# Kernel optimization log

Measured on AMD Instinct MI355X. Metric: run time of the kernel, lower is better.

Reference implementation:

```python
import jax, jax.numpy as jnp
import numpy as np

D_MODEL = 1024
NUM_HEADS = 16
D_K = D_MODEL // NUM_HEADS
B, S = 2, 2048


def setup_inputs() -> dict:
    key = jax.random.key(0)
    ks = jax.random.split(key, 9)
    sc = 1.0 / np.sqrt(D_MODEL)
    return {
        "x": jax.random.normal(ks[0], (B, S, D_MODEL), dtype=jnp.float32),
        "Wq": jax.random.normal(ks[1], (D_MODEL, D_MODEL), dtype=jnp.float32) * sc,
        "bq": jnp.zeros((D_MODEL,), dtype=jnp.float32),
        "Wk": jax.random.normal(ks[2], (D_MODEL, D_MODEL), dtype=jnp.float32) * sc,
        "bk": jnp.zeros((D_MODEL,), dtype=jnp.float32),
        "Wv": jax.random.normal(ks[3], (D_MODEL, D_MODEL), dtype=jnp.float32) * sc,
        "bv": jnp.zeros((D_MODEL,), dtype=jnp.float32),
        "Wo": jax.random.normal(ks[4], (D_MODEL, D_MODEL), dtype=jnp.float32) * sc,
        "bo": jnpp if False else jnp.zeros((D_MODEL,), dtype=jnp.float32),
    }


def reference(x, Wq, bq, Wk, bk, Wv, bv, Wo, bo):
    b, s, d = x.shape
    # projections, split heads: (B, H, S, Dk)
    def heads(t):
        return t.reshape(b, s, NUM_HEADS, D_K).transpose(0, 2, 1, 3)
    Q = heads(x @ Wq + bq)
    K = heads(x @ Wk + bk)
    V = heads(x @ Wv + bv)
    scores = jnp.einsum("bhqd,bhkd->bhqk", Q, K) / jnp.sqrt(jnp.float32(D_K))
    attn = jax.nn.softmax(scores, axis=-1)
    out = jnp.einsum("bhqk,bhkd->bhqd", attn, V)
    out = out.transpose(0, 2, 1, 3).reshape(b, s, d)
    return out @ Wo + bo
```

## Files before the change

### kernel.cpp

```cpp
#include <hip/hip_runtime.h>
#include <hip/hip_bf16.h>


#define SEQ 2048
#define DMODEL 1024
#define NHEAD 16
#define DK 64
#define NBATCH 2
#define NBH 32
#define MTOT 4096

typedef __attribute__((ext_vector_type(4))) float  f32x4;
typedef __attribute__((ext_vector_type(8))) short  bf16x8;
typedef __attribute__((ext_vector_type(4))) short  bf16x4;
typedef __attribute__((ext_vector_type(4))) unsigned short u16x4;

#define QSCALE 0.18033688f

__device__ __forceinline__ unsigned short f2bf(float x) {
  union { __hip_bfloat16 h; unsigned short u; } cv;
  cv.h = __float2bfloat16(x);
  return cv.u;
}

#define EXP2(x) __builtin_amdgcn_exp2f(x)

__device__ __forceinline__ float fmax3(float a, float b, float c) {
  return fmaxf(fmaxf(a, b), c);
}

__device__ __forceinline__ void gload16(const void* g, void* l) {
  __builtin_amdgcn_global_load_lds(
      (const __attribute__((address_space(1))) unsigned int*)g,
      (__attribute__((address_space(3))) unsigned int*)l, 16, 0, 0);
}

__global__ __launch_bounds__(256) void conv_all(
    const float* __restrict__ X, unsigned short* __restrict__ Xb,
    const float* __restrict__ W0, const float* __restrict__ W1,
    const float* __restrict__ W2, const float* __restrict__ W3,
    unsigned short* __restrict__ T0, unsigned short* __restrict__ T1,
    unsigned short* __restrict__ T2, unsigned short* __restrict__ T3) {
  __shared__ float tile[64][65];
  const int b = blockIdx.x;
  if (b >= 1024) {
    size_t i = ((size_t)(b - 1024) * 256 + threadIdx.x) * 16;
#pragma unroll
    for (int c = 0; c < 4; ++c) {
      f32x4 v = *(const f32x4*)&X[i + c * 4];
      u16x4 pk;
      pk[0] = f2bf(v[0]); pk[1] = f2bf(v[1]);
      pk[2] = f2bf(v[2]); pk[3] = f2bf(v[3]);
      *(u16x4*)&Xb[i + c * 4] = pk;
    }
    return;
  }
  const int z = b >> 8, rem = b & 255;
  const float* W; unsigned short* T;
  switch (z) {
    case 0: W = W0; T = T0; break;
    case 1: W = W1; T = T1; break;
    case 2: W = W2; T = T2; break;
    default: W = W3; T = T3; break;
  }
  const int k0 = (rem & 15) * 64, n0 = (rem >> 4) * 64;
  const int tr = threadIdx.x >> 4, tc = (threadIdx.x & 15) * 4;
#pragma unroll
  for (int i = 0; i < 4; ++i) {
    int r = tr + i * 16;
    f32x4 v = *(const f32x4*)&W[(size_t)(k0 + r) * DMODEL + n0 + tc];
    tile[r][tc + 0] = v[0]; tile[r][tc + 1] = v[1];
    tile[r][tc + 2] = v[2]; tile[r][tc + 3] = v[3];
  }
  __syncthreads();
#pragma unroll
  for (int i = 0; i < 4; ++i) {
    int nr = tr + i * 16;
    u16x4 pk;
    pk[0] = f2bf(tile[tc + 0][nr]); pk[1] = f2bf(tile[tc + 1][nr]);
    pk[2] = f2bf(tile[tc + 2][nr]); pk[3] = f2bf(tile[tc + 3][nr]);
    *(u16x4*)&T[(size_t)(n0 + nr) * DMODEL + k0 + tc] = pk;
  }
}

__global__ __launch_bounds__(256) void gemm_qkv(
    const short* __restrict__ A, const short* __restrict__ Bt,
    const float* __restrict__ bq, const float* __restrict__ bk,
    const float* __restrict__ bv, unsigned short* __restrict__ Qg,
    unsigned short* __restrict__ Kg, unsigned short* __restrict__ Vtg) {
  const int tid = threadIdx.x;
  const int lane = tid & 63, w = tid >> 6;
  const int lq = lane & 15, g = lane >> 4;
  const int m0 = blockIdx.y * 128, n0 = blockIdx.x * 128;
  const int wm = (w >> 1) * 64, wn = (w & 1) * 64;
  const int which = n0 >> 10;

  __shared__ __attribute__((aligned(16))) short abuf[128 * 64];
  __shared__ __attribute__((aligned(16))) short bbuf[128 * 64];

  f32x4 acc[4][4] = {};
  const char* Ab = (const char*)A;
  const char* Bb = (const char*)Bt;

  for (int kt = 0; kt < 16; ++kt) {
    __syncthreads();
#pragma unroll
    for (int i = 0; i < 4; ++i) {
      int y = tid * 16 + i * 4096;
      int row = y >> 7, cb = y & 127;
      gload16(Ab + (size_t)(m0 + row) * 2048 + kt * 128 + cb, (char*)abuf + y);
      gload16(Bb + (size_t)(n0 + row) * 2048 + kt * 128 + cb, (char*)bbuf + y);
    }
    __syncthreads();
#pragma unroll
    for (int ks = 0; ks < 2; ++ks) {
      bf16x8 af[4], bfr[4];
#pragma unroll
      for (int i = 0; i < 4; ++i) {
        af[i]  = *(const bf16x8*)&abuf[(wm + i * 16 + lq) * 64 + ks * 32 + g * 8];
        bfr[i] = *(const bf16x8*)&bbuf[(wn + i * 16 + lq) * 64 + ks * 32 + g * 8];
      }
#pragma unroll
      for (int mi = 0; mi < 4; ++mi)
#pragma unroll
        for (int ni = 0; ni < 4; ++ni)
          acc[mi][ni] = __builtin_amdgcn_mfma_f32_16x16x32_bf16(
              af[mi], bfr[ni], acc[mi][ni], 0, 0, 0);
    }
  }

  const float* bias = (which == 0) ? bq : (which == 1) ? bk : bv;
  unsigned short* o = (which == 0) ? Qg : (which == 1) ? Kg : Vtg;
  const float sc = (which == 0) ? QSCALE : 1.0f;

#pragma unroll
  for (int mi = 0; mi < 4; ++mi) {
#pragma unroll
    for (int ni = 0; ni < 4; ++ni) {
      const int nl = (n0 & 1023) + wn + ni * 16 + lq;
      const int mbase = m0 + wm + mi * 16 + g * 4;
      const float bs = bias[nl];
      const int h = nl >> 6, d = nl & 63;
      if (which == 2) {
        const int b = mbase >> 11, s = mbase & 2047;
        u16x4 pk;
#pragma unroll
        for (int r = 0; r < 4; ++r) pk[r] = f2bf(acc[mi][ni][r] + bs);
        *(u16x4*)&o[(size_t)((b * NHEAD + h) * DK + d) * SEQ + s] = pk;
      } else {
#pragma unroll
        for (int r = 0; r < 4; ++r) {
          const int m = mbase + r;
          const int b = m >> 11, s = m & 2047;
          o[(size_t)((b * NHEAD + h) * SEQ + s) * DK + d] =
              f2bf((acc[mi][ni][r] + bs) * sc);
        }
      }
    }
  }
}

__global__ __launch_bounds__(256) void gemm_out(const short* __restrict__ A,
                                                const short* __restrict__ Bt,
                                                const float* __restrict__ bias,
                                                float* __restrict__ o) {
  const int tid = threadIdx.x;
  const int lane = tid & 63, w = tid >> 6;
  const int lq = lane & 15, g = lane >> 4;
  const int m0 = blockIdx.y * 128, n0 = blockIdx.x * 128;
  const int wm = (w >> 1) * 64, wn = (w & 1) * 64;

  __shared__ __attribute__((aligned(16))) short abuf[128 * 64];
  __shared__ __attribute__((aligned(16))) short bbuf[128 * 64];

  f32x4 acc[4][4] = {};
  const char* Ab = (const char*)A;
  const char* Bb = (const char*)Bt;

  for (int kt = 0; kt < 16; ++kt) {
    __syncthreads();
#pragma unroll
    for (int i = 0; i < 4; ++i) {
      int y = tid * 16 + i * 4096;
      int row = y >> 7, cb = y & 127;
      gload16(Ab + (size_t)(m0 + row) * 2048 + kt * 128 + cb, (char*)abuf + y);
      gload16(Bb + (size_t)(n0 + row) * 2048 + kt * 128 + cb, (char*)bbuf + y);
    }
    __syncthreads();
#pragma unroll
    for (int ks = 0; ks < 2; ++ks) {
      bf16x8 af[4], bfr[4];
#pragma unroll
      for (int i = 0; i < 4; ++i) {
        af[i]  = *(const bf16x8*)&abuf[(wm + i * 16 + lq) * 64 + ks * 32 + g * 8];
        bfr[i] = *(const bf16x8*)&bbuf[(wn + i * 16 + lq) * 64 + ks * 32 + g * 8];
      }
#pragma unroll
      for (int mi = 0; mi < 4; ++mi)
#pragma unroll
        for (int ni = 0; ni < 4; ++ni)
          acc[mi][ni] = __builtin_amdgcn_mfma_f32_16x16x32_bf16(
              af[mi], bfr[ni], acc[mi][ni], 0, 0, 0);
    }
  }

#pragma unroll
  for (int mi = 0; mi < 4; ++mi) {
#pragma unroll
    for (int ni = 0; ni < 4; ++ni) {
      const int n = n0 + wn + ni * 16 + lq;
      const int mbase = m0 + wm + mi * 16 + g * 4;
      const float bs = bias[n];
#pragma unroll
      for (int r = 0; r < 4; ++r)
        o[(size_t)(mbase + r) * DMODEL + n] = acc[mi][ni][r] + bs;
    }
  }
}

__global__ __launch_bounds__(256) void attn_kernel(
    const short* __restrict__ Qg, const short* __restrict__ Kg,
    const short* __restrict__ Vtg, unsigned short* __restrict__ Og) {
  const int tid = threadIdx.x, lane = tid & 63, w = tid >> 6;
  const int lq = lane & 15, g = lane >> 4;
  const int bid = blockIdx.x;
  const int swz = (bid & 7) * 128 + (bid >> 3);
  const int bh = swz >> 5, q0 = (swz & 31) * 64;

  __shared__ __attribute__((aligned(16))) short kbuf[2][64 * 64];
  __shared__ __attribute__((aligned(16))) short vbuf[2][64 * 64];
  __shared__ __attribute__((aligned(16))) short pbuf[4 * 1024];

  const short* qrow = Qg + ((size_t)bh * SEQ + q0 + w * 16 + lq) * DK;
  bf16x8 qf[2];
  qf[0] = *(const bf16x8*)&qrow[g * 8];
  qf[1] = *(const bf16x8*)&qrow[32 + g * 8];

  bf16x8 ones;
#pragma unroll
  for (int j = 0; j < 8; ++j) ones[j] = (short)0x3F80;

  f32x4 oacc[4] = {};
  float m_run = -3.0e38f, l_run = 0.f;

  const char* kbase = (const char*)(Kg + (size_t)bh * SEQ * DK);
  const char* vbase = (const char*)(Vtg + (size_t)bh * DK * SEQ);
  const int sw = (lq & 7) << 4;

  const int y0 = tid * 16, y1 = y0 + 4096;
  const int r0 = y0 >> 7, r1 = y1 >> 7;
  const int c0 = (y0 ^ (r0 << 4)) & 0x70;
  const int c1 = (y1 ^ (r1 << 4)) & 0x70;
  const int ksrc0 = (y0 & ~0x70) | c0;
  const int ksrc1 = (y1 & ~0x70) | c1;
  const int vsrc0 = r0 * 4096 + c0;
  const int vsrc1 = r1 * 4096 + c1;

#define STAGE(T, BI)                                                      \
  do {                                                                    \
    gload16(kbase + (size_t)(T) * 8192 + ksrc0, (char*)kbuf[BI] + y0);    \
    gload16(kbase + (size_t)(T) * 8192 + ksrc1, (char*)kbuf[BI] + y1);    \
    gload16(vbase + vsrc0 + (size_t)(T) * 128, (char*)vbuf[BI] + y0);     \
    gload16(vbase + vsrc1 + (size_t)(T) * 128, (char*)vbuf[BI] + y1);     \
  } while (0)

  STAGE(0, 0);

  for (int t = 0; t < 32; ++t) {
    const int bi = t & 1;
    __syncthreads();
    if (t < 31) STAGE(t + 1, bi ^ 1);

    const char* kb = (const char*)kbuf[bi];
    const char* vb = (const char*)vbuf[bi];

    f32x4 sv[4];
    __builtin_amdgcn_s_setprio(1);
#pragma unroll
    for (int kt2 = 0; kt2 < 4; ++kt2) {
      f32x4 s = {};
#pragma unroll
      for (int ks = 0; ks < 2; ++ks) {
        bf16x8 kf = *(const bf16x8*)(kb + (kt2 * 16 + lq) * 128 +
                                     ((ks * 64 + g * 16) ^ sw));
        s = __builtin_amdgcn_mfma_f32_16x16x32_bf16(kf, qf[ks], s, 0, 0, 0);
      }
      sv[kt2] = s;
    }
    __builtin_amdgcn_s_setprio(0);

    float m0a = fmax3(sv[0][0], sv[0][1], sv[0][2]);
    float m1a = fmax3(sv[0][3], sv[1][0], sv[1][1]);
    float m2a = fmax3(sv[1][2], sv[1][3], sv[2][0]);
    float m3a = fmax3(sv[2][1], sv[2][2], sv[2][3]);
    float m4a = fmax3(sv[3][0], sv[3][1], sv[3][2]);
    float vmax = fmaxf(fmax3(m0a, m1a, m2a), fmax3(m3a, m4a, sv[3][3]));
    vmax = fmaxf(vmax, __shfl_xor(vmax, 16));
    vmax = fmaxf(vmax, __shfl_xor(vmax, 32));

    if (!__all(vmax <= m_run + 8.0f)) {
      const float m_new = fmaxf(m_run, vmax);
      const float corr = EXP2(m_run - m_new);
#pragma unroll
      for (int dt = 0; dt < 4; ++dt)
#pragma unroll
        for (int r = 0; r < 4; ++r) oacc[dt][r] *= corr;
      l_run *= corr;
      m_run = m_new;
    }

#pragma unroll
    for (int kt2 = 0; kt2 < 4; ++kt2)
#pragma unroll
      for (int r = 0; r < 4; ++r) sv[kt2][r] = EXP2(sv[kt2][r] - m_run);

    char* pb = (char*)pbuf + w * 2048 + lq * 128;
#pragma unroll
    for (int kt2 = 0; kt2 < 4; ++kt2) {
      bf16x4 pk;
#pragma unroll
      for (int r = 0; r < 4; ++r) pk[r] = (short)f2bf(sv[kt2][r]);
      *(bf16x4*)(pb + ((kt2 * 32 + g * 8) ^ sw)) = pk;
    }
    asm volatile("" ::: "memory");

    f32x4 lsum = {};
    __builtin_amdgcn_s_setprio(1);
#pragma unroll
    for (int ks2 = 0; ks2 < 2; ++ks2) {
      bf16x8 pf = *(const bf16x8*)(pb + ((ks2 * 64 + g * 16) ^ sw));
      lsum = __builtin_amdgcn_mfma_f32_16x16x32_bf16(ones, pf, lsum, 0, 0, 0);
#pragma unroll
      for (int dt = 0; dt < 4; ++dt) {
        bf16x8 vf = *(const bf16x8*)(vb + (dt * 16 + lq) * 128 +
                                     ((ks2 * 64 + g * 16) ^ sw));
        oacc[dt] = __builtin_amdgcn_mfma_f32_16x16x32_bf16(vf, pf, oacc[dt], 0, 0, 0);
      }
    }
    __builtin_amdgcn_s_setprio(0);
    l_run += lsum[0];
  }
#undef STAGE

  const float inv = 1.0f / l_run;
  const int b = bh >> 4, h = bh & 15;
  const size_t rowbase =
      ((size_t)b * SEQ + q0 + w * 16 + lq) * DMODEL + h * DK;
#pragma unroll
  for (int dt = 0; dt < 4; ++dt) {
    u16x4 pk;
#pragma unroll
    for (int r = 0; r < 4; ++r) pk[r] = f2bf(oacc[dt][r] * inv);
    *(u16x4*)&Og[rowbase + dt * 16 + g * 4] = pk;
  }
}

extern "C" void kernel_launch(void* const* d_in, const int* in_sizes, int n_in,
                              void* d_out, int out_size, void* d_ws,
                              size_t ws_size, hipStream_t stream) {
  const float* x  = (const float*)d_in[0];
  const float* Wq = (const float*)d_in[1];
  const float* bq = (const float*)d_in[2];
  const float* Wk = (const float*)d_in[3];
  const float* bk = (const float*)d_in[4];
  const float* Wv = (const float*)d_in[5];
  const float* bv = (const float*)d_in[6];
  const float* Wo = (const float*)d_in[7];
  const float* bo = (const float*)d_in[8];
  float* out = (float*)d_out;

  char* ws = (char*)d_ws;
  unsigned short* Xb    = (unsigned short*)(ws);
  unsigned short* Wtqkv = (unsigned short*)(ws + (8u << 20));
  unsigned short* Wto   = (unsigned short*)(ws + (14u << 20));
  unsigned short* Qg    = (unsigned short*)(ws + (16u << 20));
  unsigned short* Kg    = (unsigned short*)(ws + (24u << 20));
  unsigned short* Vtg   = (unsigned short*)(ws + (32u << 20));
  unsigned short* Ab    = Xb;

  conv_all<<<dim3(2048), 256, 0, stream>>>(
      x, Xb, Wq, Wk, Wv, Wo,
      Wtqkv, Wtqkv + (1u << 20), Wtqkv + (2u << 20), Wto);

  gemm_qkv<<<dim3(24, 32), 256, 0, stream>>>(
      (const short*)Xb, (const short*)Wtqkv, bq, bk, bv, Qg, Kg, Vtg);

  attn_kernel<<<dim3(1024), 256, 0, stream>>>(
      (const short*)Qg, (const short*)Kg, (const short*)Vtg, Ab);

  gemm_out<<<dim3(8, 32), 256, 0, stream>>>(
      (const short*)Ab, (const short*)Wto, bo, out);
}
```

Before: 148.2 us.

## Process two 16-row query tiles per wave in attention kernel

Each wave now handles 32 query rows as two 16-row tiles that share every K and V fragment read from LDS, so each block covers 128 queries and the grid halves to 512 blocks. This halves the K/V global-to-LDS staging traffic per query and the LDS reads per MFMA, and gives each wave more independent MFMAs to interleave. In exchange it roughly doubles accumulator and score register use, which may lower occupancy. With 512 blocks on a 256-CU device, fewer waves are available to hide latency.

```diff
diff --git a/kernel.cpp b/kernel.cpp
--- a/kernel.cpp
+++ b/kernel.cpp
@@ -224,24 +224,28 @@
   const int tid = threadIdx.x, lane = tid & 63, w = tid >> 6;
   const int lq = lane & 15, g = lane >> 4;
   const int bid = blockIdx.x;
-  const int swz = (bid & 7) * 128 + (bid >> 3);
-  const int bh = swz >> 5, q0 = (swz & 31) * 64;
+  const int swz = (bid & 7) * 64 + (bid >> 3);
+  const int bh = swz >> 4, q0 = (swz & 15) * 128;
 
   __shared__ __attribute__((aligned(16))) short kbuf[2][64 * 64];
   __shared__ __attribute__((aligned(16))) short vbuf[2][64 * 64];
-  __shared__ __attribute__((aligned(16))) short pbuf[4 * 1024];
-
-  const short* qrow = Qg + ((size_t)bh * SEQ + q0 + w * 16 + lq) * DK;
-  bf16x8 qf[2];
-  qf[0] = *(const bf16x8*)&qrow[g * 8];
-  qf[1] = *(const bf16x8*)&qrow[32 + g * 8];
+  __shared__ __attribute__((aligned(16))) short pbuf[4 * 2048];
+
+  const short* qrow0 = Qg + ((size_t)bh * SEQ + q0 + w * 32 + lq) * DK;
+  const short* qrow1 = qrow0 + 16 * DK;
+  bf16x8 qf0[2], qf1[2];
+  qf0[0] = *(const bf16x8*)&qrow0[g * 8];
+  qf0[1] = *(const bf16x8*)&qrow0[32 + g * 8];
+  qf1[0] = *(const bf16x8*)&qrow1[g * 8];
+  qf1[1] = *(const bf16x8*)&qrow1[32 + g * 8];
 
   bf16x8 ones;
 #pragma unroll
   for (int j = 0; j < 8; ++j) ones[j] = (short)0x3F80;
 
-  f32x4 oacc[4] = {};
-  float m_run = -3.0e38f, l_run = 0.f;
+  f32x4 oacc0[4] = {}, oacc1[4] = {};
+  float m_run0 = -3.0e38f, l_run0 = 0.f;
+  float m_run1 = -3.0e38f, l_run1 = 0.f;
 
   const char* kbase = (const char*)(Kg + (size_t)bh * SEQ * DK);
   const char* vbase = (const char*)(Vtg + (size_t)bh * DK * SEQ);
@@ -266,6 +270,9 @@
 
   STAGE(0, 0);
 
+  char* pb0 = (char*)pbuf + w * 4096 + lq * 128;
+  char* pb1 = pb0 + 2048;
+
   for (int t = 0; t < 32; ++t) {
     const int bi = t & 1;
     __syncthreads();
@@ -274,84 +281,124 @@
     const char* kb = (const char*)kbuf[bi];
     const char* vb = (const char*)vbuf[bi];
 
-    f32x4 sv[4];
+    f32x4 sv0[4], sv1[4];
     __builtin_amdgcn_s_setprio(1);
 #pragma unroll
     for (int kt2 = 0; kt2 < 4; ++kt2) {
-      f32x4 s = {};
+      f32x4 s0 = {}, s1 = {};
 #pragma unroll
       for (int ks = 0; ks < 2; ++ks) {
         bf16x8 kf = *(const bf16x8*)(kb + (kt2 * 16 + lq) * 128 +
                                      ((ks * 64 + g * 16) ^ sw));
-        s = __builtin_amdgcn_mfma_f32_16x16x32_bf16(kf, qf[ks], s, 0, 0, 0);
-      }
-      sv[kt2] = s;
+        s0 = __builtin_amdgcn_mfma_f32_16x16x32_bf16(kf, (ks ? qf0[1] : qf0[0]), s0, 0, 0, 0);
+        s1 = __builtin_amdgcn_mfma_f32_16x16x32_bf16(kf, (ks ? qf1[1] : qf1[0]), s1, 0, 0, 0);
+      }
+      sv0[kt2] = s0;
+      sv1[kt2] = s1;
     }
     __builtin_amdgcn_s_setprio(0);
 
-    float m0a = fmax3(sv[0][0], sv[0][1], sv[0][2]);
-    float m1a = fmax3(sv[0][3], sv[1][0], sv[1][1]);
-    float m2a = fmax3(sv[1][2], sv[1][3], sv[2][0]);
-    float m3a = fmax3(sv[2][1], sv[2][2], sv[2][3]);
-    float m4a = fmax3(sv[3][0], sv[3][1], sv[3][2]);
-    float vmax = fmaxf(fmax3(m0a, m1a, m2a), fmax3(m3a, m4a, sv[3][3]));
-    vmax = fmaxf(vmax, __shfl_xor(vmax, 16));
-    vmax = fmaxf(vmax, __shfl_xor(vmax, 32));
-
-    if (!__all(vmax <= m_run + 8.0f)) {
-      const float m_new = fmaxf(m_run, vmax);
-      const float corr = EXP2(m_run - m_new);
+    float a0 = fmax3(sv0[0][0], sv0[0][1], sv0[0][2]);
+    float a1 = fmax3(sv0[0][3], sv0[1][0], sv0[1][1]);
+    float a2 = fmax3(sv0[1][2], sv0[1][3], sv0[2][0]);
+    float a3 = fmax3(sv0[2][1], sv0[2][2], sv0[2][3]);
+    float a4 = fmax3(sv0[3][0], sv0[3][1], sv0[3][2]);
+    float vmax0 = fmaxf(fmax3(a0, a1, a2), fmax3(a3, a4, sv0[3][3]));
+    float b0 = fmax3(sv1[0][0], sv1[0][1], sv1[0][2]);
+    float b1 = fmax3(sv1[0][3], sv1[1][0], sv1[1][1]);
+    float b2 = fmax3(sv1[1][2], sv1[1][3], sv1[2][0]);
+    float b3 = fmax3(sv1[2][1], sv1[2][2], sv1[2][3]);
+    float b4 = fmax3(sv1[3][0], sv1[3][1], sv1[3][2]);
+    float vmax1 = fmaxf(fmax3(b0, b1, b2), fmax3(b3, b4, sv1[3][3]));
+    vmax0 = fmaxf(vmax0, __shfl_xor(vmax0, 16));
+    vmax0 = fmaxf(vmax0, __shfl_xor(vmax0, 32));
+    vmax1 = fmaxf(vmax1, __shfl_xor(vmax1, 16));
+    vmax1 = fmaxf(vmax1, __shfl_xor(vmax1, 32));
+
+    const bool ok = (vmax0 <= m_run0 + 8.0f) && (vmax1 <= m_run1 + 8.0f);
+    if (!__all(ok)) {
+      const float mn0 = fmaxf(m_run0, vmax0);
+      const float cr0 = EXP2(m_run0 - mn0);
+      const float mn1 = fmaxf(m_run1, vmax1);
+      const float cr1 = EXP2(m_run1 - mn1);
 #pragma unroll
       for (int dt = 0; dt < 4; ++dt)
 #pragma unroll
-        for (int r = 0; r < 4; ++r) oacc[dt][r] *= corr;
-      l_run *= corr;
-      m_run = m_new;
+        for (int r = 0; r < 4; ++r) {
+          oacc0[dt][r] *= cr0;
+          oacc1[dt][r] *= cr1;
+        }
+      l_run0 *= cr0; m_run0 = mn0;
+      l_run1 *= cr1; m_run1 = mn1;
     }
 
 #pragma unroll
     for (int kt2 = 0; kt2 < 4; ++kt2)
 #pragma unroll
-      for (int r = 0; r < 4; ++r) sv[kt2][r] = EXP2(sv[kt2][r] - m_run);
-
-    char* pb = (char*)pbuf + w * 2048 + lq * 128;
+      for (int r = 0; r < 4; ++r) {
+        sv0[kt2][r] = EXP2(sv0[kt2][r] - m_run0);
+        sv1[kt2][r] = EXP2(sv1[kt2][r] - m_run1);
+      }
+
 #pragma unroll
     for (int kt2 = 0; kt2 < 4; ++kt2) {
-      bf16x4 pk;
-#pragma unroll
-      for (int r = 0; r < 4; ++r) pk[r] = (short)f2bf(sv[kt2][r]);
-      *(bf16x4*)(pb + ((kt2 * 32 + g * 8) ^ sw)) = pk;
+      bf16x4 pk0, pk1;
+#pragma unroll
+      for (int r = 0; r < 4; ++r) {
+        pk0[r] = (short)f2bf(sv0[kt2][r]);
+        pk1[r] = (short)f2bf(sv1[kt2][r]);
+      }
+      *(bf16x4*)(pb0 + ((kt2 * 32 + g * 8) ^ sw)) = pk0;
+      *(bf16x4*)(pb1 + ((kt2 * 32 + g * 8) ^ sw)) = pk1;
     }
     asm volatile("" ::: "memory");
 
-    f32x4 lsum = {};
+    f32x4 lsum0 = {}, lsum1 = {};
     __builtin_amdgcn_s_setprio(1);
 #pragma unroll
     for (int ks2 = 0; ks2 < 2; ++ks2) {
-      bf16x8 pf = *(const bf16x8*)(pb + ((ks2 * 64 + g * 16) ^ sw));
-      lsum = __builtin_amdgcn_mfma_f32_16x16x32_bf16(ones, pf, lsum, 0, 0, 0);
+      bf16x8 pf0 = *(const bf16x8*)(pb0 + ((ks2 * 64 + g * 16) ^ sw));
+      bf16x8 pf1 = *(const bf16x8*)(pb1 + ((ks2 * 64 + g * 16) ^ sw));
+      lsum0 = __builtin_amdgcn_mfma_f32_16x16x32_bf16(ones, pf0, lsum0, 0, 0, 0);
+      lsum1 = __builtin_amdgcn_mfma_f32_16x16x32_bf16(ones, pf1, lsum1, 0, 0, 0);
 #pragma unroll
       for (int dt = 0; dt < 4; ++dt) {
         bf16x8 vf = *(const bf16x8*)(vb + (dt * 16 + lq) * 128 +
                                      ((ks2 * 64 + g * 16) ^ sw));
-        oacc[dt] = __builtin_amdgcn_mfma_f32_16x16x32_bf16(vf, pf, oacc[dt], 0, 0, 0);
+        oacc0[dt] = __builtin_amdgcn_mfma_f32_16x16x32_bf16(vf, pf0, oacc0[dt], 0, 0, 0);
+        oacc1[dt] = __builtin_amdgcn_mfma_f32_16x16x32_bf16(vf, pf1, oacc1[dt], 0, 0, 0);
       }
     }
     __builtin_amdgcn_s_setprio(0);
-    l_run += lsum[0];
+    l_run0 += lsum0[0];
+    l_run1 += lsum1[0];
   }
 #undef STAGE
 
-  const float inv = 1.0f / l_run;
   const int b = bh >> 4, h = bh & 15;
-  const size_t rowbase =
-      ((size_t)b * SEQ + q0 + w * 16 + lq) * DMODEL + h * DK;
-#pragma unroll
-  for (int dt = 0; dt < 4; ++dt) {
-    u16x4 pk;
-#pragma unroll
-    for (int r = 0; r < 4; ++r) pk[r] = f2bf(oacc[dt][r] * inv);
-    *(u16x4*)&Og[rowbase + dt * 16 + g * 4] = pk;
+  {
+    const float inv = 1.0f / l_run0;
+    const size_t rowbase =
+        ((size_t)b * SEQ + q0 + w * 32 + lq) * DMODEL + h * DK;
+#pragma unroll
+    for (int dt = 0; dt < 4; ++dt) {
+      u16x4 pk;
+#pragma unroll
+      for (int r = 0; r < 4; ++r) pk[r] = f2bf(oacc0[dt][r] * inv);
+      *(u16x4*)&Og[rowbase + dt * 16 + g * 4] = pk;
+    }
+  }
+  {
+    const float inv = 1.0f / l_run1;
+    const size_t rowbase =
+        ((size_t)b * SEQ + q0 + w * 32 + 16 + lq) * DMODEL + h * DK;
+#pragma unroll
+    for (int dt = 0; dt < 4; ++dt) {
+      u16x4 pk;
+#pragma unroll
+      for (int r = 0; r < 4; ++r) pk[r] = f2bf(oacc1[dt][r] * inv);
+      *(u16x4*)&Og[rowbase + dt * 16 + g * 4] = pk;
+    }
   }
 }
 
@@ -385,7 +432,7 @@
   gemm_qkv<<<dim3(24, 32), 256, 0, stream>>>(
       (const short*)Xb, (const short*)Wtqkv, bq, bk, bv, Qg, Kg, Vtg);
 
-  attn_kernel<<<dim3(1024), 256, 0, stream>>>(
+  attn_kernel<<<dim3(512), 256, 0, stream>>>(
       (const short*)Qg, (const short*)Kg, (const short*)Vtg, Ab);
 
   gemm_out<<<dim3(8, 32), 256, 0, stream>>>(
```

Result: no change. 150.0 us (+1.2%).

## Switch attention to 32x32x16 MFMA with 128-query blocks and remap GEMM grids

Applied to the files above, without the earlier changes.

The attention kernel now uses 32x32x16 bf16 MFMA tiles. Each wave handles 32 query rows instead of 16, and each block covers 128 queries, which halves the block count and the K/V tile reloads per query. The row max now needs only one cross-half shuffle. The QKV and output GEMMs move to 1D grids with a custom block-to-tile mapping, meant to improve L2 locality. The trade-off is higher register pressure from the 16-wide accumulators and fewer blocks to fill the GPU.

```diff
diff --git a/kernel.cpp b/kernel.cpp
--- a/kernel.cpp
+++ b/kernel.cpp
@@ -10,10 +10,11 @@
 #define NBH 32
 #define MTOT 4096
 
-typedef __attribute__((ext_vector_type(4))) float  f32x4;
-typedef __attribute__((ext_vector_type(8))) short  bf16x8;
-typedef __attribute__((ext_vector_type(4))) short  bf16x4;
-typedef __attribute__((ext_vector_type(4))) unsigned short u16x4;
+typedef __attribute__((ext_vector_type(4)))  float  f32x4;
+typedef __attribute__((ext_vector_type(16))) float  f32x16;
+typedef __attribute__((ext_vector_type(8)))  short  bf16x8;
+typedef __attribute__((ext_vector_type(4)))  short  bf16x4;
+typedef __attribute__((ext_vector_type(4)))  unsigned short u16x4;
 
 #define QSCALE 0.18033688f
 
@@ -91,7 +92,10 @@
   const int tid = threadIdx.x;
   const int lane = tid & 63, w = tid >> 6;
   const int lq = lane & 15, g = lane >> 4;
-  const int m0 = blockIdx.y * 128, n0 = blockIdx.x * 128;
+  const int bidg = blockIdx.x;
+  const int j = bidg >> 3;
+  const int n_t = (bidg & 7) * 3 + (j % 3);
+  const int m0 = (j / 3) * 128, n0 = n_t * 128;
   const int wm = (w >> 1) * 64, wn = (w & 1) * 64;
   const int which = n0 >> 10;
 
@@ -167,7 +171,7 @@
   const int tid = threadIdx.x;
   const int lane = tid & 63, w = tid >> 6;
   const int lq = lane & 15, g = lane >> 4;
-  const int m0 = blockIdx.y * 128, n0 = blockIdx.x * 128;
+  const int m0 = (blockIdx.x >> 3) * 128, n0 = (blockIdx.x & 7) * 128;
   const int wm = (w >> 1) * 64, wn = (w & 1) * 64;
 
   __shared__ __attribute__((aligned(16))) short abuf[128 * 64];
@@ -222,30 +226,31 @@
     const short* __restrict__ Qg, const short* __restrict__ Kg,
     const short* __restrict__ Vtg, unsigned short* __restrict__ Og) {
   const int tid = threadIdx.x, lane = tid & 63, w = tid >> 6;
-  const int lq = lane & 15, g = lane >> 4;
+  const int l5 = lane & 31, hi = lane >> 5;
+  const int sw7 = l5 & 7, hi8 = hi * 8;
   const int bid = blockIdx.x;
-  const int swz = (bid & 7) * 128 + (bid >> 3);
-  const int bh = swz >> 5, q0 = (swz & 31) * 64;
+  const int swz = (bid & 7) * 64 + (bid >> 3);
+  const int bh = swz >> 4, q0 = (swz & 15) * 128;
 
   __shared__ __attribute__((aligned(16))) short kbuf[2][64 * 64];
   __shared__ __attribute__((aligned(16))) short vbuf[2][64 * 64];
-  __shared__ __attribute__((aligned(16))) short pbuf[4 * 1024];
-
-  const short* qrow = Qg + ((size_t)bh * SEQ + q0 + w * 16 + lq) * DK;
-  bf16x8 qf[2];
-  qf[0] = *(const bf16x8*)&qrow[g * 8];
-  qf[1] = *(const bf16x8*)&qrow[32 + g * 8];
+  __shared__ __attribute__((aligned(16))) short pbuf[4][32 * 64];
+
+  const short* qrow = Qg + ((size_t)bh * SEQ + q0 + w * 32 + l5) * DK;
+  bf16x8 qf[4];
+#pragma unroll
+  for (int ds = 0; ds < 4; ++ds)
+    qf[ds] = *(const bf16x8*)&qrow[ds * 16 + hi8];
 
   bf16x8 ones;
 #pragma unroll
-  for (int j = 0; j < 8; ++j) ones[j] = (short)0x3F80;
-
-  f32x4 oacc[4] = {};
+  for (int jj = 0; jj < 8; ++jj) ones[jj] = (short)0x3F80;
+
+  f32x16 oacc0 = {}, oacc1 = {};
   float m_run = -3.0e38f, l_run = 0.f;
 
   const char* kbase = (const char*)(Kg + (size_t)bh * SEQ * DK);
   const char* vbase = (const char*)(Vtg + (size_t)bh * DK * SEQ);
-  const int sw = (lq & 7) << 4;
 
   const int y0 = tid * 16, y1 = y0 + 4096;
   const int r0 = y0 >> 7, r1 = y1 >> 7;
@@ -266,6 +271,8 @@
 
   STAGE(0, 0);
 
+  char* pb = (char*)&pbuf[w][0] + l5 * 128;
+
   for (int t = 0; t < 32; ++t) {
     const int bi = t & 1;
     __syncthreads();
@@ -274,84 +281,94 @@
     const char* kb = (const char*)kbuf[bi];
     const char* vb = (const char*)vbuf[bi];
 
-    f32x4 sv[4];
+    f32x16 s0 = {}, s1 = {};
     __builtin_amdgcn_s_setprio(1);
 #pragma unroll
-    for (int kt2 = 0; kt2 < 4; ++kt2) {
-      f32x4 s = {};
-#pragma unroll
-      for (int ks = 0; ks < 2; ++ks) {
-        bf16x8 kf = *(const bf16x8*)(kb + (kt2 * 16 + lq) * 128 +
-                                     ((ks * 64 + g * 16) ^ sw));
-        s = __builtin_amdgcn_mfma_f32_16x16x32_bf16(kf, qf[ks], s, 0, 0, 0);
+    for (int ds = 0; ds < 4; ++ds) {
+      const int ch = ((ds * 2 + hi) ^ sw7) << 4;
+      bf16x8 kf0 = *(const bf16x8*)(kb + l5 * 128 + ch);
+      bf16x8 kf1 = *(const bf16x8*)(kb + (32 + l5) * 128 + ch);
+      s0 = __builtin_amdgcn_mfma_f32_32x32x16_bf16(kf0, qf[ds], s0, 0, 0, 0);
+      s1 = __builtin_amdgcn_mfma_f32_32x32x16_bf16(kf1, qf[ds], s1, 0, 0, 0);
+    }
+    __builtin_amdgcn_s_setprio(0);
+
+    float t0 = fmax3(s0[0], s0[1], s0[2]);
+    float t1 = fmax3(s0[3], s0[4], s0[5]);
+    float t2 = fmax3(s0[6], s0[7], s0[8]);
+    float t3 = fmax3(s0[9], s0[10], s0[11]);
+    float t4 = fmax3(s0[12], s0[13], s0[14]);
+    float t5 = fmax3(s1[0], s1[1], s1[2]);
+    float t6 = fmax3(s1[3], s1[4], s1[5]);
+    float t7 = fmax3(s1[6], s1[7], s1[8]);
+    float t8 = fmax3(s1[9], s1[10], s1[11]);
+    float t9 = fmax3(s1[12], s1[13], s1[14]);
+    float u0 = fmax3(t0, t1, t2);
+    float u1 = fmax3(t3, t4, s0[15]);
+    float u2 = fmax3(t5, t6, t7);
+    float u3 = fmax3(t8, t9, s1[15]);
+    float lm = fmaxf(fmax3(u0, u1, u2), u3);
+
+    if (!__all(lm <= m_run + 8.0f)) {
+      float vm = fmaxf(lm, __shfl_xor(lm, 32));
+      const float mn = fmaxf(m_run, vm);
+      const float cr = EXP2(m_run - mn);
+#pragma unroll
+      for (int r = 0; r < 16; ++r) { oacc0[r] *= cr; oacc1[r] *= cr; }
+      l_run *= cr;
+      m_run = mn;
+    }
+
+#pragma unroll
+    for (int r = 0; r < 16; ++r) {
+      s0[r] = EXP2(s0[r] - m_run);
+      s1[r] = EXP2(s1[r] - m_run);
+    }
+
+#pragma unroll
+    for (int c = 0; c < 4; ++c) {
+      bf16x4 pk0, pk1;
+#pragma unroll
+      for (int b = 0; b < 4; ++b) {
+        pk0[b] = (short)f2bf(s0[4 * c + b]);
+        pk1[b] = (short)f2bf(s1[4 * c + b]);
       }
-      sv[kt2] = s;
+      *(bf16x4*)(pb + ((c ^ sw7) << 4) + hi8) = pk0;
+      *(bf16x4*)(pb + (((4 + c) ^ sw7) << 4) + hi8) = pk1;
+    }
+    asm volatile("" ::: "memory");
+
+    f32x16 ls = {};
+    __builtin_amdgcn_s_setprio(1);
+#pragma unroll
+    for (int ks = 0; ks < 4; ++ks) {
+      const int ch = ((ks * 2 + hi) ^ sw7) << 4;
+      bf16x8 pf = *(const bf16x8*)(pb + ch);
+      ls = __builtin_amdgcn_mfma_f32_32x32x16_bf16(ones, pf, ls, 0, 0, 0);
+      bf16x8 vf0 = *(const bf16x8*)(vb + l5 * 128 + ch);
+      bf16x8 vf1 = *(const bf16x8*)(vb + (32 + l5) * 128 + ch);
+      oacc0 = __builtin_amdgcn_mfma_f32_32x32x16_bf16(vf0, pf, oacc0, 0, 0, 0);
+      oacc1 = __builtin_amdgcn_mfma_f32_32x32x16_bf16(vf1, pf, oacc1, 0, 0, 0);
     }
     __builtin_amdgcn_s_setprio(0);
-
-    float m0a = fmax3(sv[0][0], sv[0][1], sv[0][2]);
-    float m1a = fmax3(sv[0][3], sv[1][0], sv[1][1]);
-    float m2a = fmax3(sv[1][2], sv[1][3], sv[2][0]);
-    float m3a = fmax3(sv[2][1], sv[2][2], sv[2][3]);
-    float m4a = fmax3(sv[3][0], sv[3][1], sv[3][2]);
-    float vmax = fmaxf(fmax3(m0a, m1a, m2a), fmax3(m3a, m4a, sv[3][3]));
-    vmax = fmaxf(vmax, __shfl_xor(vmax, 16));
-    vmax = fmaxf(vmax, __shfl_xor(vmax, 32));
-
-    if (!__all(vmax <= m_run + 8.0f)) {
-      const float m_new = fmaxf(m_run, vmax);
-      const float corr = EXP2(m_run - m_new);
-#pragma unroll
-      for (int dt = 0; dt < 4; ++dt)
-#pragma unroll
-        for (int r = 0; r < 4; ++r) oacc[dt][r] *= corr;
-      l_run *= corr;
-      m_run = m_new;
-    }
-
-#pragma unroll
-    for (int kt2 = 0; kt2 < 4; ++kt2)
-#pragma unroll
-      for (int r = 0; r < 4; ++r) sv[kt2][r] = EXP2(sv[kt2][r] - m_run);
-
-    char* pb = (char*)pbuf + w * 2048 + lq * 128;
-#pragma unroll
-    for (int kt2 = 0; kt2 < 4; ++kt2) {
-      bf16x4 pk;
-#pragma unroll
-      for (int r = 0; r < 4; ++r) pk[r] = (short)f2bf(sv[kt2][r]);
-      *(bf16x4*)(pb + ((kt2 * 32 + g * 8) ^ sw)) = pk;
-    }
-    asm volatile("" ::: "memory");
-
-    f32x4 lsum = {};
-    __builtin_amdgcn_s_setprio(1);
-#pragma unroll
-    for (int ks2 = 0; ks2 < 2; ++ks2) {
-      bf16x8 pf = *(const bf16x8*)(pb + ((ks2 * 64 + g * 16) ^ sw));
-      lsum = __builtin_amdgcn_mfma_f32_16x16x32_bf16(ones, pf, lsum, 0, 0, 0);
-#pragma unroll
-      for (int dt = 0; dt < 4; ++dt) {
-        bf16x8 vf = *(const bf16x8*)(vb + (dt * 16 + lq) * 128 +
-                                     ((ks2 * 64 + g * 16) ^ sw));
-        oacc[dt] = __builtin_amdgcn_mfma_f32_16x16x32_bf16(vf, pf, oacc[dt], 0, 0, 0);
-      }
-    }
-    __builtin_amdgcn_s_setprio(0);
-    l_run += lsum[0];
+    l_run += ls[0];
   }
 #undef STAGE
 
   const float inv = 1.0f / l_run;
-  const int b = bh >> 4, h = bh & 15;
-  const size_t rowbase =
-      ((size_t)b * SEQ + q0 + w * 16 + lq) * DMODEL + h * DK;
-#pragma unroll
-  for (int dt = 0; dt < 4; ++dt) {
-    u16x4 pk;
-#pragma unroll
-    for (int r = 0; r < 4; ++r) pk[r] = f2bf(oacc[dt][r] * inv);
-    *(u16x4*)&Og[rowbase + dt * 16 + g * 4] = pk;
+  const int bb = bh >> 4, h = bh & 15;
+  const size_t base =
+      ((size_t)bb * SEQ + q0 + w * 32 + l5) * DMODEL + h * DK + hi * 4;
+#pragma unroll
+  for (int c = 0; c < 4; ++c) {
+    u16x4 pk0, pk1;
+#pragma unroll
+    for (int b = 0; b < 4; ++b) {
+      pk0[b] = f2bf(oacc0[4 * c + b] * inv);
+      pk1[b] = f2bf(oacc1[4 * c + b] * inv);
+    }
+    *(u16x4*)&Og[base + 8 * c] = pk0;
+    *(u16x4*)&Og[base + 32 + 8 * c] = pk1;
   }
 }
 
@@ -382,12 +399,12 @@
       x, Xb, Wq, Wk, Wv, Wo,
       Wtqkv, Wtqkv + (1u << 20), Wtqkv + (2u << 20), Wto);
 
-  gemm_qkv<<<dim3(24, 32), 256, 0, stream>>>(
+  gemm_qkv<<<dim3(768), 256, 0, stream>>>(
       (const short*)Xb, (const short*)Wtqkv, bq, bk, bv, Qg, Kg, Vtg);
 
-  attn_kernel<<<dim3(1024), 256, 0, stream>>>(
+  attn_kernel<<<dim3(512), 256, 0, stream>>>(
       (const short*)Qg, (const short*)Kg, (const short*)Vtg, Ab);
 
-  gemm_out<<<dim3(8, 32), 256, 0, stream>>>(
+  gemm_out<<<dim3(256), 256, 0, stream>>>(
       (const short*)Ab, (const short*)Wto, bo, out);
 }
```

Measured after the change: 142.2 us. 4.0% less time.
